# Optimization experiments

Measured on AMD Instinct MI355X. Metric: run time of the kernel, lower is better.

The kernel has to match this reference:

```python
import jax, jax.numpy as jnp
import numpy as np

B, T, D, H = 4, 2048, 1024, 8
HD = D // H  # head_dim = 128


def setup_inputs() -> dict:
    key = jax.random.key(0)
    ks = jax.random.split(key, 10)
    s = 1.0 / np.sqrt(D)
    return {
        "x": jax.random.normal(ks[0], (B, T, D), jnp.float32),
        "y": jax.random.normal(ks[1], (B, T, D), jnp.float32),
        "Wq": jax.random.normal(ks[2], (D, D), jnp.float32) * s,
        "bq": jnp.zeros((D,), jnp.float32),
        "Wk": jax.random.normal(ks[3], (D, D), jnp.float32) * s,
        "bk": jnp.zeros((D,), jnp.float32),
        "Wv": jax.random.normal(ks[4], (D, D), jnp.float32) * s,
        "bv": jnp.zeros((D,), jnp.float32),
        "Wo": jax.random.normal(ks[5], (D, D), jnp.float32) * s,
        "bo": jnp.zeros((D,), jnp.float32),
    }


def _heads(t):
    # [B, T, D] -> [B, H, T, HD]
    b, t_, _ = t.shape
    return t.reshape(b, t_, H, HD).transpose(0, 2, 1, 3)


def reference(x, y, Wq, bq, Wk, bk, Wv, bv, Wo, bo):
    Tq, Tk = x.shape[1], y.shape[1]
    q = _heads(x @ Wq.T + bq)  # [B,H,Tq,HD]
    k = _heads(y @ Wk.T + bk)  # [B,H,Tk,HD]
    v = _heads(y @ Wv.T + bv)  # [B,H,Tk,HD]
    scale = 1.0 / np.sqrt(HD)
    logits = jnp.einsum("bhqd,bhkd->bhqk", q, k) * scale
    # causal mask: positions k > q get -inf
    causal = jnp.triu(jnp.full((Tq, Tk), -jnp.inf, jnp.float32), k=1)
    logits = logits + causal
    attn = jax.nn.softmax(logits, axis=-1)  # [B,H,Tq,Tk]
    ctx = jnp.einsum("bhqk,bhkd->bhqd", attn, v)
    ctx = ctx.transpose(0, 2, 1, 3).reshape(x.shape[0], Tq, D)
    out = ctx @ Wo.T + bo
    return out
```

## Files before the change

### kernel.cpp

```cpp
#include <hip/hip_runtime.h>
#include <math.h>

#define TB 4
#define TT 2048
#define TD 1024
#define TH 8
#define THD 128

typedef __attribute__((ext_vector_type(8))) short short8;
typedef __attribute__((ext_vector_type(4))) short short4v;
typedef __attribute__((ext_vector_type(4))) float float4v;
typedef __attribute__((ext_vector_type(16))) float float16v;

__device__ __forceinline__ short f2bf(float f) {
    union { float f; unsigned u; } v; v.f = f;
    unsigned r = v.u + 0x7FFFu + ((v.u >> 16) & 1u);
    return (short)(r >> 16);
}

__device__ __forceinline__ float bf2f(short s) {
    union { unsigned u; float f; } v;
    v.u = ((unsigned)(unsigned short)s) << 16;
    return v.f;
}

__device__ __forceinline__ short8 cvt8(float4v a, float4v b) {
    short8 r;
    r[0] = f2bf(a[0]); r[1] = f2bf(a[1]); r[2] = f2bf(a[2]); r[3] = f2bf(a[3]);
    r[4] = f2bf(b[0]); r[5] = f2bf(b[1]); r[6] = f2bf(b[2]); r[7] = f2bf(b[3]);
    return r;
}

__device__ __forceinline__ void async16(const void* g, void* l) {
    __builtin_amdgcn_global_load_lds(
        (const __attribute__((address_space(1))) unsigned int*)g,
        (__attribute__((address_space(3))) unsigned int*)l, 16, 0, 0);
}

__global__ void cvtall(const float* __restrict__ x, const float* __restrict__ y,
                       const float* __restrict__ wq, const float* __restrict__ wk,
                       const float* __restrict__ wv, const float* __restrict__ wo,
                       short* __restrict__ xyb, short* __restrict__ wb)
{
    const size_t SZ = (size_t)TB * TT * TD;
    const size_t WSZ = (size_t)TD * TD;
    int ty = blockIdx.y;
    const float* s; short* d; size_t n;
    if (ty == 0)      { s = x;  d = xyb;      n = SZ; }
    else if (ty == 1) { s = y;  d = xyb + SZ; n = SZ; }
    else {
        s = (ty == 2) ? wq : (ty == 3) ? wk : (ty == 4) ? wv : wo;
        d = wb + (size_t)(ty - 2) * WSZ; n = WSZ;
    }
    size_t i = ((size_t)blockIdx.x * blockDim.x + threadIdx.x) * 8;
    if (i >= n) return;
    float4v v0 = *(const float4v*)(s + i);
    float4v v1 = *(const float4v*)(s + i + 4);
    *(short8*)(d + i) = cvt8(v0, v1);
}

__device__ __forceinline__ void gemm_core256(const short* __restrict__ A,
                                             const short* __restrict__ W,
                                             int m0, int n0, short* SM,
                                             float4v acc[4][4])
{
    short* As = SM;
    short* Bs = SM + 32768;
    const int tid = threadIdx.x;
    const int lane = tid & 63, wid = tid >> 6;
    const int lr = lane & 15, qd = lane >> 4, sw = lane & 7;
    const int wr = wid >> 1, wc = wid & 1;
    const int rsub = lane >> 3;
    const int gj = ((lane & 7) ^ rsub) * 8;
    const int K = TD;

    const short* aSrc[4]; int aDst[4];
    const short* bSrc[2]; int bDst[2];
#pragma unroll
    for (int p = 0; p < 4; ++p) {
        int ch = wid * 4 + p;
        aSrc[p] = A + (size_t)(m0 + ch * 8 + rsub) * K + gj;
        aDst[p] = ch * 512;
    }
#pragma unroll
    for (int p = 0; p < 2; ++p) {
        int ch = wid * 2 + p;
        bSrc[p] = W + (size_t)(n0 + ch * 8 + rsub) * K + gj;
        bDst[p] = ch * 512;
    }

#pragma unroll
    for (int mt = 0; mt < 4; ++mt)
#pragma unroll
        for (int nt = 0; nt < 4; ++nt)
            acc[mt][nt] = float4v{0.f, 0.f, 0.f, 0.f};

#pragma unroll
    for (int t = 0; t < 2; ++t) {
#pragma unroll
        for (int p = 0; p < 4; ++p)
            async16(aSrc[p] + t * 64, As + t * 16384 + aDst[p]);
#pragma unroll
        for (int p = 0; p < 2; ++p)
            async16(bSrc[p] + t * 64, Bs + t * 8192 + bDst[p]);
    }
    asm volatile("s_waitcnt vmcnt(6)" ::: "memory");
    __builtin_amdgcn_sched_barrier(0);
    __builtin_amdgcn_s_barrier();

#pragma unroll 2
    for (int it = 0; it < 16; ++it) {
        const short* Ac = As + (it & 1) * 16384;
        const short* Bc = Bs + (it & 1) * 8192;
        short* Asn = As + (it & 1) * 16384;
        short* Bsn = Bs + (it & 1) * 8192;
        const int kb2 = (it + 2) * 64;
        const bool stg = (it < 14);

        short8 af[4][2], bf[4][2];

#pragma unroll
        for (int mi = 0; mi < 2; ++mi)
#pragma unroll
            for (int ks = 0; ks < 2; ++ks)
                af[mi][ks] = *(const short8*)&Ac[(wr * 64 + mi * 16 + lr) * 64 +
                                                 (((ks * 4 + qd) ^ sw) * 8)];
#pragma unroll
        for (int ni = 0; ni < 2; ++ni)
#pragma unroll
            for (int ks = 0; ks < 2; ++ks)
                bf[ni][ks] = *(const short8*)&Bc[(wc * 64 + ni * 16 + lr) * 64 +
                                                 (((ks * 4 + qd) ^ sw) * 8)];
        asm volatile("s_waitcnt lgkmcnt(0)" ::: "memory");
        __builtin_amdgcn_sched_barrier(0);
        __builtin_amdgcn_s_setprio(1);
#pragma unroll
        for (int mi = 0; mi < 2; ++mi)
#pragma unroll
            for (int ni = 0; ni < 2; ++ni)
#pragma unroll
                for (int ks = 0; ks < 2; ++ks)
                    acc[mi][ni] = __builtin_amdgcn_mfma_f32_16x16x32_bf16(
                        af[mi][ks], bf[ni][ks], acc[mi][ni], 0, 0, 0);
        __builtin_amdgcn_s_setprio(0);
        __builtin_amdgcn_sched_barrier(0);
        __builtin_amdgcn_s_barrier();

#pragma unroll
        for (int mi = 2; mi < 4; ++mi)
#pragma unroll
            for (int ks = 0; ks < 2; ++ks)
                af[mi][ks] = *(const short8*)&Ac[(wr * 64 + mi * 16 + lr) * 64 +
                                                 (((ks * 4 + qd) ^ sw) * 8)];
        asm volatile("s_waitcnt lgkmcnt(0)" ::: "memory");
        __builtin_amdgcn_sched_barrier(0);
        __builtin_amdgcn_s_setprio(1);
#pragma unroll
        for (int mi = 2; mi < 4; ++mi)
#pragma unroll
            for (int ni = 0; ni < 2; ++ni)
#pragma unroll
                for (int ks = 0; ks < 2; ++ks)
                    acc[mi][ni] = __builtin_amdgcn_mfma_f32_16x16x32_bf16(
                        af[mi][ks], bf[ni][ks], acc[mi][ni], 0, 0, 0);
        __builtin_amdgcn_s_setprio(0);
        __builtin_amdgcn_sched_barrier(0);
        __builtin_amdgcn_s_barrier();

        if (stg) {
#pragma unroll
            for (int p = 0; p < 4; ++p)
                async16(aSrc[p] + kb2, Asn + aDst[p]);
        }
#pragma unroll
        for (int ni = 2; ni < 4; ++ni)
#pragma unroll
            for (int ks = 0; ks < 2; ++ks)
                bf[ni][ks] = *(const short8*)&Bc[(wc * 64 + ni * 16 + lr) * 64 +
                                                 (((ks * 4 + qd) ^ sw) * 8)];
        asm volatile("s_waitcnt lgkmcnt(0)" ::: "memory");
        __builtin_amdgcn_sched_barrier(0);
        __builtin_amdgcn_s_setprio(1);
#pragma unroll
        for (int mi = 2; mi < 4; ++mi)
#pragma unroll
            for (int ni = 2; ni < 4; ++ni)
#pragma unroll
                for (int ks = 0; ks < 2; ++ks)
                    acc[mi][ni] = __builtin_amdgcn_mfma_f32_16x16x32_bf16(
                        af[mi][ks], bf[ni][ks], acc[mi][ni], 0, 0, 0);
        __builtin_amdgcn_s_setprio(0);
        __builtin_amdgcn_sched_barrier(0);
        __builtin_amdgcn_s_barrier();

        if (stg) {
#pragma unroll
            for (int p = 0; p < 2; ++p)
                async16(bSrc[p] + kb2, Bsn + bDst[p]);
        }
        __builtin_amdgcn_s_setprio(1);
#pragma unroll
        for (int mi = 0; mi < 2; ++mi)
#pragma unroll
            for (int ni = 2; ni < 4; ++ni)
#pragma unroll
                for (int ks = 0; ks < 2; ++ks)
                    acc[mi][ni] = __builtin_amdgcn_mfma_f32_16x16x32_bf16(
                        af[mi][ks], bf[ni][ks], acc[mi][ni], 0, 0, 0);
        __builtin_amdgcn_s_setprio(0);
        if (stg) { asm volatile("s_waitcnt vmcnt(6)" ::: "memory"); }
        else     { asm volatile("s_waitcnt vmcnt(0)" ::: "memory"); }
        __builtin_amdgcn_sched_barrier(0);
        __builtin_amdgcn_s_barrier();
    }
}

__global__ __launch_bounds__(512, 2)
void gemm_qkv8(const short* __restrict__ xyb, const short* __restrict__ wb,
               const float* __restrict__ bq, const float* __restrict__ bk,
               const float* __restrict__ bv,
               short* __restrict__ qhp, short* __restrict__ khp,
               short* __restrict__ vtp)
{
    __shared__ __attribute__((aligned(16))) short SM[49152];
    const size_t SZ = (size_t)TB * TT * TD;
    const int bid = blockIdx.x;
    const int lin = (bid & 7) * 96 + (bid >> 3);
    const int by = lin / 24, bx = lin - by * 24;
    const int mode = bx >> 3;
    const int n0 = (bx & 7) * 128;
    const int h_ = n0 >> 7;
    const int m0 = by * 256;
    const short* A = (mode == 0) ? xyb : (xyb + SZ);
    const short* W = wb + (size_t)mode * TD * TD;
    const float* bias = (mode == 0) ? bq : (mode == 1) ? bk : bv;
    const float scale = (mode == 0)
        ? (0.08838834764831845f * 1.4426950408889634f) : 1.0f;

    float4v acc[4][4];
    gemm_core256(A, W, m0, n0, SM, acc);

    const int tid = threadIdx.x;
    const int lane = tid & 63, wid = tid >> 6;
    const int lr = lane & 15, qd = lane >> 4;
    const int wr = wid >> 1, wc = wid & 1;

#pragma unroll
    for (int nt = 0; nt < 4; ++nt) {
        int col = wc * 64 + nt * 16 + lr;
        float bi = bias[n0 + col];
#pragma unroll
        for (int mt = 0; mt < 4; ++mt)
#pragma unroll
            for (int i = 0; i < 4; ++i) {
                int row = wr * 64 + mt * 16 + qd * 4 + i;
                short v = f2bf((acc[mt][nt][i] + bi) * scale);
                if (mode < 2) SM[row * 128 + col] = v;
                else          SM[col * 264 + row] = v;
            }
    }
    __syncthreads();

    if (mode < 2) {
        short* outp = (mode == 0) ? qhp : khp;
#pragma unroll
        for (int r8 = 0; r8 < 8; ++r8) {
            int row = r8 * 32 + (tid >> 4), c = tid & 15;
            short8 v = *(const short8*)&SM[row * 128 + c * 8];
            int tg = m0 + row;
            int b_ = tg >> 11, t_ = tg & (TT - 1);
            *(short8*)&outp[(((size_t)(b_ * TH + h_)) * TT + t_) * THD + c * 8] = v;
        }
    } else {
        int b_ = m0 >> 11, t0 = m0 & (TT - 1);
#pragma unroll
        for (int r8 = 0; r8 < 8; ++r8) {
            int hd = r8 * 16 + (tid >> 5), c = tid & 31;
            short8 v = *(const short8*)&SM[hd * 264 + c * 8];
            *(short8*)&vtp[(((size_t)(b_ * TH + h_)) * THD + hd) * TT + t0 + c * 8] = v;
        }
    }
}

__global__ __launch_bounds__(512, 2)
void gemm_out8(const short* __restrict__ A, const short* __restrict__ W,
               const float* __restrict__ bias, float* __restrict__ outp)
{
    __shared__ __attribute__((aligned(16))) short SM[49152];
    const int bid = blockIdx.x;
    const int lin = (bid & 7) * 32 + (bid >> 3);
    const int by = lin >> 3, bx = lin & 7;
    const int m0 = by * 256, n0 = bx * 128;

    float4v acc[4][4];
    gemm_core256(A, W, m0, n0, SM, acc);

    const int tid = threadIdx.x;
    const int lane = tid & 63, wid = tid >> 6;
    const int lr = lane & 15, qd = lane >> 4;
    const int wr = wid >> 1, wc = wid & 1;
#pragma unroll
    for (int nt = 0; nt < 4; ++nt) {
        int col = n0 + wc * 64 + nt * 16 + lr;
        float bi = bias[col];
#pragma unroll
        for (int mt = 0; mt < 4; ++mt)
#pragma unroll
            for (int i = 0; i < 4; ++i) {
                int row = m0 + wr * 64 + mt * 16 + qd * 4 + i;
                outp[(size_t)row * TD + col] = acc[mt][nt][i] + bi;
            }
    }
}

__global__ __launch_bounds__(256, 2)
void attn_fwd(const short* __restrict__ qh, const short* __restrict__ kh,
              const short* __restrict__ vt, short* __restrict__ po,
              float* __restrict__ pl)
{
    __shared__ __attribute__((aligned(16))) short Ks[2][64 * 128];
    __shared__ __attribute__((aligned(16))) short Vs[2][128 * 64];

    const int tid = threadIdx.x;
    const int lane = tid & 63, wid = tid >> 6;
    const int l31 = lane & 31, h = lane >> 5;
    const int sw7 = l31 & 7;

    const int bi = blockIdx.x;
    const int bh = bi & 31;
    const int j  = bi >> 5;
    const size_t bho = (size_t)bh * TT * THD;

    for (int u = 0; u < 2; ++u) {
        const int qt  = u ? (15 - j) : j;
        const int kv0 = u ? (qt + 1) : 0;
        const int kv1 = u ? (2 * qt + 2) : (j + 1);

        short8 qf[8];
        {
            const short* qp = qh + bho + (size_t)(qt * 128 + wid * 32 + l31) * THD;
#pragma unroll
            for (int ks = 0; ks < 8; ++ks)
                qf[ks] = *(const short8*)(qp + ks * 16 + h * 8);
        }
        float16v o[4];
#pragma unroll
        for (int db = 0; db < 4; ++db)
#pragma unroll
            for (int r = 0; r < 16; ++r) o[db][r] = 0.f;
        float li = 0.f;

        {
            const short* kbase = kh + bho + (size_t)kv0 * 64 * THD;
            const short* vbase = vt + (size_t)bh * THD * TT + (size_t)kv0 * 64;
#pragma unroll
            for (int p = 0; p < 4; ++p) {
                int ch = wid * 4 + p;
                int kr = ch * 4 + (lane >> 4);
                int kg = (lane & 15) ^ (kr & 7);
                async16(kbase + (size_t)kr * THD + kg * 8, &Ks[0][ch * 512]);
                int vr = ch * 8 + (lane >> 3);
                int vg = (lane & 7) ^ (vr & 7);
                async16(vbase + (size_t)vr * TT + vg * 8, &Vs[0][ch * 512]);
            }
        }
        __syncthreads();

        int cur = 0;
        for (int kv = kv0; kv < kv1; ++kv) {
            if (kv + 1 < kv1) {
                const short* kbase = kh + bho + (size_t)(kv + 1) * 64 * THD;
                const short* vbase = vt + (size_t)bh * THD * TT +
                                     (size_t)(kv + 1) * 64;
#pragma unroll
                for (int p = 0; p < 4; ++p) {
                    int ch = wid * 4 + p;
                    int kr = ch * 4 + (lane >> 4);
                    int kg = (lane & 15) ^ (kr & 7);
                    async16(kbase + (size_t)kr * THD + kg * 8,
                            &Ks[cur ^ 1][ch * 512]);
                    int vr = ch * 8 + (lane >> 3);
                    int vg = (lane & 7) ^ (vr & 7);
                    async16(vbase + (size_t)vr * TT + vg * 8,
                            &Vs[cur ^ 1][ch * 512]);
                }
            }

            const short* Kc = Ks[cur];
            const short* Vc = Vs[cur];

            float16v s[2];
#pragma unroll
            for (int kb = 0; kb < 2; ++kb)
#pragma unroll
                for (int r = 0; r < 16; ++r) s[kb][r] = 0.f;
#pragma unroll
            for (int ks = 0; ks < 8; ++ks) {
                int cidx = ((ks * 2 + h) ^ sw7) * 8;
                short8 kf0 = *(const short8*)&Kc[l31 * 128 + cidx];
                short8 kf1 = *(const short8*)&Kc[(32 + l31) * 128 + cidx];
                s[0] = __builtin_amdgcn_mfma_f32_32x32x16_bf16(kf0, qf[ks], s[0], 0, 0, 0);
                s[1] = __builtin_amdgcn_mfma_f32_32x32x16_bf16(kf1, qf[ks], s[1], 0, 0, 0);
            }

            if (kv >= 2 * qt) {
                int q = qt * 128 + wid * 32 + l31;
#pragma unroll
                for (int r = 0; r < 16; ++r) {
                    int key = kv * 64 + (r & 3) + 8 * (r >> 2) + 4 * h;
                    if (key > q) s[0][r] = -1e30f;
                    if (key + 32 > q) s[1][r] = -1e30f;
                }
            }

#pragma unroll
            for (int st = 0; st < 8; ++st) {
                float e0 = exp2f(s[st >> 2][(st & 3) * 4 + 0]);
                float e1 = exp2f(s[st >> 2][(st & 3) * 4 + 1]);
                float e2 = exp2f(s[st >> 2][(st & 3) * 4 + 2]);
                float e3 = exp2f(s[st >> 2][(st & 3) * 4 + 3]);
                li += (e0 + e1) + (e2 + e3);
                short4v ap;
                ap[0] = f2bf(e0); ap[1] = f2bf(e1);
                ap[2] = f2bf(e2); ap[3] = f2bf(e3);
#pragma unroll
                for (int db = 0; db < 4; ++db) {
                    short4v vf = *(const short4v*)&Vc[(db * 32 + l31) * 64 +
                                                      ((st ^ sw7) * 8) + h * 4];
                    o[db] = __builtin_amdgcn_mfma_f32_32x32x8bf16_1k(ap, vf, o[db], 0, 0, 0);
                }
            }
            __syncthreads();
            cur ^= 1;
        }

        li += __shfl_xor(li, 32);
        const int slot = (bh * 16 + qt) * 2 + u;
        if (h == 0) pl[slot * 128 + wid * 32 + l31] = li;
        short* pop = po + (size_t)slot * 16384 + (size_t)(wid * 32) * 128 + l31;
#pragma unroll
        for (int r = 0; r < 16; ++r) {
            int ql = (r & 3) + 8 * (r >> 2) + 4 * h;
#pragma unroll
            for (int db = 0; db < 4; ++db)
                pop[(size_t)ql * 128 + db * 32] = f2bf(o[db][r]);
        }
    }
}

__global__ __launch_bounds__(256)
void combine(const short* __restrict__ po, const float* __restrict__ pl,
             short* __restrict__ ctx)
{
    const unsigned i = blockIdx.x * 256 + threadIdx.x;
    const int hdv = i & 15;
    const int q   = (i >> 4) & 127;
    const int qt  = (i >> 11) & 15;
    const int bh  = i >> 15;
    const int tile = bh * 16 + qt;
    const size_t base = (size_t)tile * 2 * 16384 + (size_t)q * 128 + hdv * 8;
    short8 a = *(const short8*)&po[base];
    short8 b = *(const short8*)&po[base + 16384];
    const float inv = 1.f / (pl[tile * 2 * 128 + q] + pl[(tile * 2 + 1) * 128 + q]);
    short8 r;
#pragma unroll
    for (int k = 0; k < 8; ++k)
        r[k] = f2bf((bf2f(a[k]) + bf2f(b[k])) * inv);
    const int b_ = bh >> 3, h_ = bh & 7, t = qt * 128 + q;
    *(short8*)&ctx[((size_t)(b_ * TT + t)) * TD + h_ * THD + hdv * 8] = r;
}

extern "C" void kernel_launch(void* const* d_in, const int* in_sizes, int n_in,
                              void* d_out, int out_size, void* d_ws, size_t ws_size,
                              hipStream_t stream) {
    (void)in_sizes; (void)n_in; (void)out_size; (void)ws_size;
    const float* x  = (const float*)d_in[0];
    const float* y  = (const float*)d_in[1];
    const float* Wq = (const float*)d_in[2];
    const float* bq = (const float*)d_in[3];
    const float* Wk = (const float*)d_in[4];
    const float* bk = (const float*)d_in[5];
    const float* Wv = (const float*)d_in[6];
    const float* bv = (const float*)d_in[7];
    const float* Wo = (const float*)d_in[8];
    const float* bo = (const float*)d_in[9];
    float* out = (float*)d_out;

    const size_t SZ = (size_t)TB * TT * TD;
    const size_t WSZ = (size_t)TD * TD;
    short* xyb = (short*)d_ws;
    short* wb  = xyb + 2 * SZ;
    short* qh  = wb + 4 * WSZ;
    short* kh  = qh + SZ;
    short* vt  = kh + SZ;
    float* pl  = (float*)(vt + SZ);
    short* po  = xyb;
    short* ctx = qh;

    hipLaunchKernelGGL(cvtall, dim3(SZ / 2048, 6), dim3(256), 0, stream,
                       x, y, Wq, Wk, Wv, Wo, xyb, wb);
    hipLaunchKernelGGL(gemm_qkv8, dim3(768), dim3(512), 0, stream,
                       xyb, wb, bq, bk, bv, qh, kh, vt);
    hipLaunchKernelGGL(attn_fwd, dim3(512), dim3(256), 0, stream, qh, kh, vt, po, pl);
    hipLaunchKernelGGL(combine, dim3(4096), dim3(256), 0, stream, po, pl, ctx);
    hipLaunchKernelGGL(gemm_out8, dim3(256), dim3(512), 0, stream,
                       ctx, wb + 3 * WSZ, bo, out);
}
```

Measured before the change: 290.6 us.

## Restructure GEMM main loop into two phases with overlapped LDS fragment loads

Rewrites the inner K-loop of the GEMM from four load/compute phases with four barriers into two phases with two barriers. All A fragments and all B fragments are loaded up front. A partial lgkmcnt wait lets the first half of the MFMAs start while the second B half is still arriving. Both A and B async global prefetches are then issued together after one barrier. The aim is fewer workgroup barriers and more overlap between LDS reads and MFMA, at the cost of higher register pressure from holding every fragment live at once.

```diff
diff --git a/kernel.cpp b/kernel.cpp
--- a/kernel.cpp
+++ b/kernel.cpp
@@ -120,7 +120,7 @@
         short8 af[4][2], bf[4][2];
 
 #pragma unroll
-        for (int mi = 0; mi < 2; ++mi)
+        for (int mi = 0; mi < 4; ++mi)
 #pragma unroll
             for (int ks = 0; ks < 2; ++ks)
                 af[mi][ks] = *(const short8*)&Ac[(wr * 64 + mi * 16 + lr) * 64 +
@@ -131,11 +131,18 @@
             for (int ks = 0; ks < 2; ++ks)
                 bf[ni][ks] = *(const short8*)&Bc[(wc * 64 + ni * 16 + lr) * 64 +
                                                  (((ks * 4 + qd) ^ sw) * 8)];
-        asm volatile("s_waitcnt lgkmcnt(0)" ::: "memory");
+        __builtin_amdgcn_sched_barrier(0);
+#pragma unroll
+        for (int ni = 2; ni < 4; ++ni)
+#pragma unroll
+            for (int ks = 0; ks < 2; ++ks)
+                bf[ni][ks] = *(const short8*)&Bc[(wc * 64 + ni * 16 + lr) * 64 +
+                                                 (((ks * 4 + qd) ^ sw) * 8)];
+        asm volatile("s_waitcnt lgkmcnt(4)" ::: "memory");
         __builtin_amdgcn_sched_barrier(0);
         __builtin_amdgcn_s_setprio(1);
 #pragma unroll
-        for (int mi = 0; mi < 2; ++mi)
+        for (int mi = 0; mi < 4; ++mi)
 #pragma unroll
             for (int ni = 0; ni < 2; ++ni)
 #pragma unroll
@@ -144,63 +151,22 @@
                         af[mi][ks], bf[ni][ks], acc[mi][ni], 0, 0, 0);
         __builtin_amdgcn_s_setprio(0);
         __builtin_amdgcn_sched_barrier(0);
+        asm volatile("s_waitcnt lgkmcnt(0)" ::: "memory");
+        __builtin_amdgcn_sched_barrier(0);
         __builtin_amdgcn_s_barrier();
-
-#pragma unroll
-        for (int mi = 2; mi < 4; ++mi)
-#pragma unroll
-            for (int ks = 0; ks < 2; ++ks)
-                af[mi][ks] = *(const short8*)&Ac[(wr * 64 + mi * 16 + lr) * 64 +
-                                                 (((ks * 4 + qd) ^ sw) * 8)];
-        asm volatile("s_waitcnt lgkmcnt(0)" ::: "memory");
-        __builtin_amdgcn_sched_barrier(0);
-        __builtin_amdgcn_s_setprio(1);
-#pragma unroll
-        for (int mi = 2; mi < 4; ++mi)
-#pragma unroll
-            for (int ni = 0; ni < 2; ++ni)
-#pragma unroll
-                for (int ks = 0; ks < 2; ++ks)
-                    acc[mi][ni] = __builtin_amdgcn_mfma_f32_16x16x32_bf16(
-                        af[mi][ks], bf[ni][ks], acc[mi][ni], 0, 0, 0);
-        __builtin_amdgcn_s_setprio(0);
-        __builtin_amdgcn_sched_barrier(0);
-        __builtin_amdgcn_s_barrier();
+        __builtin_amdgcn_sched_barrier(0);
 
         if (stg) {
 #pragma unroll
             for (int p = 0; p < 4; ++p)
                 async16(aSrc[p] + kb2, Asn + aDst[p]);
-        }
-#pragma unroll
-        for (int ni = 2; ni < 4; ++ni)
-#pragma unroll
-            for (int ks = 0; ks < 2; ++ks)
-                bf[ni][ks] = *(const short8*)&Bc[(wc * 64 + ni * 16 + lr) * 64 +
-                                                 (((ks * 4 + qd) ^ sw) * 8)];
-        asm volatile("s_waitcnt lgkmcnt(0)" ::: "memory");
-        __builtin_amdgcn_sched_barrier(0);
-        __builtin_amdgcn_s_setprio(1);
-#pragma unroll
-        for (int mi = 2; mi < 4; ++mi)
-#pragma unroll
-            for (int ni = 2; ni < 4; ++ni)
-#pragma unroll
-                for (int ks = 0; ks < 2; ++ks)
-                    acc[mi][ni] = __builtin_amdgcn_mfma_f32_16x16x32_bf16(
-                        af[mi][ks], bf[ni][ks], acc[mi][ni], 0, 0, 0);
-        __builtin_amdgcn_s_setprio(0);
-        __builtin_amdgcn_sched_barrier(0);
-        __builtin_amdgcn_s_barrier();
-
-        if (stg) {
 #pragma unroll
             for (int p = 0; p < 2; ++p)
                 async16(bSrc[p] + kb2, Bsn + bDst[p]);
         }
         __builtin_amdgcn_s_setprio(1);
 #pragma unroll
-        for (int mi = 0; mi < 2; ++mi)
+        for (int mi = 0; mi < 4; ++mi)
 #pragma unroll
             for (int ni = 2; ni < 4; ++ni)
 #pragma unroll
```

Measured after the change: 277.0 us, median of 2. 4.7% less time.
